# Kernel optimization log

Measured on AMD Instinct MI355X. Metric: run time of the kernel, lower is better.

The kernel has to match this reference:

```python
import jax, jax.numpy as jnp
import numpy as np

N_EMBD = 1024
HIDDEN = 4 * N_EMBD          # 4096
ADAPT = HIDDEN // 16         # 256
NUM_EXPERTS = 8
B, S = 4, 2048
LN_EPS = 1e-5


def setup_inputs() -> dict:
    key = jax.random.key(0)
    ks = jax.random.split(key, 8)
    x = jax.random.normal(ks[0], (B, S, N_EMBD), dtype=jnp.float32)
    # top-1 routing: one-hot expert weights (disjoint masks, standard MoE dispatch)
    route = jax.random.randint(ks[1], (B, S), 0, NUM_EXPERTS)
    expert_weights = jax.nn.one_hot(route, NUM_EXPERTS, dtype=jnp.float32)
    up_scale = 0.1 / N_EMBD ** 0.5
    adapt_scale0 = 0.1 / HIDDEN ** 0.5
    adapt_scale = 0.01 / ADAPT ** 0.5
    W_up = jax.random.normal(ks[2], (HIDDEN, N_EMBD), dtype=jnp.float32) * up_scale
    W_adapt = jax.random.normal(ks[3], (ADAPT, HIDDEN), dtype=jnp.float32) * adapt_scale0
    W_exp_adapters = jax.random.normal(ks[4], (NUM_EXPERTS, ADAPT, ADAPT), dtype=jnp.float32) * adapt_scale
    ln_gamma = jnp.ones((NUM_EXPERTS, ADAPT), dtype=jnp.float32)
    ln_beta = jnp.zeros((NUM_EXPERTS, ADAPT), dtype=jnp.float32)
    W_expert_proj = jax.random.normal(ks[5], (HIDDEN, ADAPT), dtype=jnp.float32) * adapt_scale
    W_out = jax.random.normal(ks[6], (N_EMBD, HIDDEN), dtype=jnp.float32) * adapt_scale
    return {"x": x, "expert_weights": expert_weights, "W_up": W_up,
            "W_adapt": W_adapt, "W_exp_adapters": W_exp_adapters,
            "ln_gamma": ln_gamma, "ln_beta": ln_beta,
            "W_expert_proj": W_expert_proj, "W_out": W_out}


def reference(x, expert_weights, W_up, W_adapt, W_exp_adapters, ln_gamma, ln_beta, W_expert_proj, W_out):
    b, s, d = x.shape
    T = b * s
    E = expert_weights.shape[-1]
    xt = x.reshape(T, d)

    # shared MLP path (silu(up_proj(x))) -> output_proj
    h = jax.nn.silu(xt @ W_up.T)                      # [T, HIDDEN]
    shared_out = (h @ W_out.T).reshape(b, s, d)       # [B, S, D]

    active = expert_weights.reshape(T, E) > 0         # [T, E]
    any_active = jnp.any(active, axis=-1)             # [T]
    last_idx = E - 1 - jnp.argmax(active[:, ::-1], axis=-1)  # [T]

    # pre_adapt (silu(up) recomputed == h) -> adapt_proj
    a = h @ W_adapt.T                                 # [T, ADAPT]
    # per-expert adapter linears, then select the winning expert per token
    a_all = jnp.einsum('td,eod->teo', a, W_exp_adapters)      # [T, E, ADAPT]
    a_sel = jnp.take_along_axis(a_all, last_idx[:, None, None], axis=1)[:, 0]  # [T, ADAPT]

    # per-expert LayerNorm params gathered per token
    g = ln_gamma[last_idx]                            # [T, ADAPT]
    be = ln_beta[last_idx]
    mu = jnp.mean(a_sel, axis=-1, keepdims=True)
    var = jnp.mean(jnp.square(a_sel - mu), axis=-1, keepdims=True)
    a_norm = (a_sel - mu) * jax.lax.rsqrt(var + LN_EPS) * g + be

    h2 = a_norm @ W_expert_proj.T                     # [T, HIDDEN]
    e_out = h2 @ W_out.T                              # [T, D]
    combined = jnp.where(any_active[:, None], e_out, 0.0).reshape(b, s, d)
    return shared_out + 0.1 * combined
```

## Files before the change

### kernel.cpp

```cpp
#include <hip/hip_runtime.h>
#include <cstdint>

#define TOK  8192
#define DEMB 1024
#define HID  4096
#define ADP  256
#define NEXP 8
#define KAUG 4352

typedef __bf16 bf16x8 __attribute__((ext_vector_type(8)));
typedef float  f32x4  __attribute__((ext_vector_type(4)));

__device__ __forceinline__ unsigned short f2bf(float f) {
  unsigned int u = __float_as_uint(f);
  u += 0x7fffu + ((u >> 16) & 1u);
  return (unsigned short)(u >> 16);
}
__device__ __forceinline__ float bf2f(unsigned short b) {
  return __uint_as_float(((unsigned int)b) << 16);
}

__global__ __launch_bounds__(256) void convert_all(
    const float* __restrict__ x, const float* __restrict__ wup,
    const float* __restrict__ wout, const float* __restrict__ wadapt,
    const float* __restrict__ wexp, const float* __restrict__ ew,
    unsigned short* __restrict__ xb, unsigned short* __restrict__ wub,
    unsigned short* __restrict__ wob, unsigned short* __restrict__ wab,
    unsigned short* __restrict__ web, int* __restrict__ route) {
  int b = blockIdx.x;
  if (b >= 8960) {
    int t = (b - 8960) * 256 + threadIdx.x;
    const float* p = ew + (size_t)t * NEXP;
    int r = -1;
#pragma unroll
    for (int e = 0; e < NEXP; ++e)
      if (p[e] > 0.f) r = e;
    route[t] = r;
    return;
  }
  const float* src; unsigned short* dst; int lb; bool strided = false;
  if      (b < 4096) { src = x;      dst = xb;  lb = b; }
  else if (b < 6144) { src = wup;    dst = wub; lb = b - 4096; }
  else if (b < 8192) { src = wout;   dst = wob; lb = b - 6144; strided = true; }
  else if (b < 8704) { src = wadapt; dst = wab; lb = b - 8192; }
  else               { src = wexp;   dst = web; lb = b - 8704; }
  size_t base = (size_t)lb * 2048;
#pragma unroll
  for (int h = 0; h < 2; ++h) {
    size_t off = base + (size_t)h * 1024 + (size_t)threadIdx.x * 4;
    float4 v = *(const float4*)(src + off);
    ushort4 o;
    o.x = f2bf(v.x); o.y = f2bf(v.y); o.z = f2bf(v.z); o.w = f2bf(v.w);
    size_t doff = strided ? (off >> 12) * KAUG + (off & 4095) : off;
    *(ushort4*)(dst + doff) = o;
  }
}

__global__ __launch_bounds__(256) void wp_transpose(
    const float* __restrict__ wp, unsigned short* __restrict__ wpT) {
  __shared__ float tile[64][65];
  const int h0 = blockIdx.x * 64;
  const int a0 = blockIdx.y * 64;
  const int t = threadIdx.x;
  const int r = t >> 4;
  const int c = (t & 15) * 4;
#pragma unroll
  for (int p = 0; p < 4; ++p) {
    int row = p * 16 + r;
    float4 v = *(const float4*)(wp + (size_t)(h0 + row) * ADP + a0 + c);
    tile[c + 0][row] = v.x;
    tile[c + 1][row] = v.y;
    tile[c + 2][row] = v.z;
    tile[c + 3][row] = v.w;
  }
  __syncthreads();
#pragma unroll
  for (int q = 0; q < 2; ++q) {
    int idx = q * 256 + t;
    int al = idx >> 3;
    int hg = (idx & 7) * 8;
    unsigned int w0 = (unsigned int)f2bf(tile[al][hg + 0]) |
                      ((unsigned int)f2bf(tile[al][hg + 1]) << 16);
    unsigned int w1 = (unsigned int)f2bf(tile[al][hg + 2]) |
                      ((unsigned int)f2bf(tile[al][hg + 3]) << 16);
    unsigned int w2 = (unsigned int)f2bf(tile[al][hg + 4]) |
                      ((unsigned int)f2bf(tile[al][hg + 5]) << 16);
    unsigned int w3 = (unsigned int)f2bf(tile[al][hg + 6]) |
                      ((unsigned int)f2bf(tile[al][hg + 7]) << 16);
    uint4 o = make_uint4(w0, w1, w2, w3);
    *(uint4*)(wpT + (size_t)(a0 + al) * HID + h0 + hg) = o;
  }
}

__device__ __forceinline__ void stage_tile(const unsigned short* __restrict__ g,
                                           int ldg, unsigned short* lds,
                                           int wave, int lane) {
  int srow = lane >> 3;
  int scol = ((lane & 7) ^ (srow & 7)) * 8;
#pragma unroll
  for (int c = 0; c < 4; ++c) {
    int chunk = wave * 4 + c;
    const unsigned short* gp = g + (size_t)(chunk * 8 + srow) * ldg + scol;
    unsigned short* lp = lds + chunk * 512;
    __builtin_amdgcn_global_load_lds(
        (const __attribute__((address_space(1))) unsigned int*)(uintptr_t)gp,
        (__attribute__((address_space(3))) unsigned int*)(uintptr_t)lp,
        16, 0, 0);
  }
}

template <int EPI>
__global__ __launch_bounds__(256) void gemm128(
    const unsigned short* __restrict__ A, int lda,
    const unsigned short* __restrict__ B, int ldb,
    void* __restrict__ C, int ldc,
    const int* __restrict__ route, int kLen, long splitStride) {
  __shared__ unsigned short As[128 * 64];
  __shared__ unsigned short Bs[128 * 64];
  const int lane = threadIdx.x & 63;
  const int wave = threadIdx.x >> 6;
  const int wm = wave >> 1, wn = wave & 1;
  const long rowBase = (long)blockIdx.y * 128;
  const long colBase = (long)blockIdx.x * 128;
  const int ks = blockIdx.z * kLen;
  const unsigned short* Ap = A + rowBase * lda + ks;
  const unsigned short* Bp = B + colBase * ldb + ks;
  f32x4 acc[4][4] = {};

  for (int kt = 0; kt < kLen; kt += 64) {
    stage_tile(Ap + kt, lda, As, wave, lane);
    stage_tile(Bp + kt, ldb, Bs, wave, lane);
    __syncthreads();
#pragma unroll
    for (int kk = 0; kk < 64; kk += 32) {
      const int kb = (kk >> 3) + (lane >> 4);
      const int sw = kb ^ (lane & 7);
      bf16x8 af[4], bfr[4];
#pragma unroll
      for (int mt = 0; mt < 4; ++mt) {
        int m = wm * 64 + mt * 16 + (lane & 15);
        af[mt] = *(const bf16x8*)&As[m * 64 + sw * 8];
      }
#pragma unroll
      for (int nt = 0; nt < 4; ++nt) {
        int n = wn * 64 + nt * 16 + (lane & 15);
        bfr[nt] = *(const bf16x8*)&Bs[n * 64 + sw * 8];
      }
#pragma unroll
      for (int mt = 0; mt < 4; ++mt)
#pragma unroll
        for (int nt = 0; nt < 4; ++nt)
          acc[mt][nt] = __builtin_amdgcn_mfma_f32_16x16x32_bf16(
              af[mt], bfr[nt], acc[mt][nt], 0, 0, 0);
    }
    __syncthreads();
  }

  const int rsub = (lane >> 4) * 4;
  const int csub = lane & 15;
#pragma unroll
  for (int mt = 0; mt < 4; ++mt) {
#pragma unroll
    for (int nt = 0; nt < 4; ++nt) {
      long col = colBase + wn * 64 + nt * 16 + csub;
#pragma unroll
      for (int r = 0; r < 4; ++r) {
        long row = rowBase + wm * 64 + mt * 16 + rsub + r;
        float v = acc[mt][nt][r];
        if (EPI == 0) {
          float s = __fdividef(v, 1.0f + __expf(-v));
          ((unsigned short*)C)[row * ldc + col] = f2bf(s);
        } else if (EPI == 1) {
          ((float*)C + splitStride * blockIdx.z)[row * ldc + col] = v;
        } else {
          if (route[row] == (int)(col >> 8))
            ((float*)C)[row * ADP + (col & 255)] = v;
        }
      }
    }
  }
}

__global__ __launch_bounds__(256) void reduce_cast(
    const float* __restrict__ P, unsigned short* __restrict__ ab) {
  size_t i = ((size_t)blockIdx.x * 256 + threadIdx.x) * 4;
  const size_t stride = (size_t)TOK * ADP;
  float4 p0 = *(const float4*)(P + i);
  float4 p1 = *(const float4*)(P + stride + i);
  float4 p2 = *(const float4*)(P + 2 * stride + i);
  float4 p3 = *(const float4*)(P + 3 * stride + i);
  ushort4 o;
  o.x = f2bf(p0.x + p1.x + p2.x + p3.x);
  o.y = f2bf(p0.y + p1.y + p2.y + p3.y);
  o.z = f2bf(p0.z + p1.z + p2.z + p3.z);
  o.w = f2bf(p0.w + p1.w + p2.w + p3.w);
  *(ushort4*)(ab + i) = o;
}

__global__ __launch_bounds__(256) void wcomb_reduce(
    const float* __restrict__ Pw, unsigned short* __restrict__ wob) {
  size_t i = ((size_t)blockIdx.x * 256 + threadIdx.x) * 4;
  const size_t stride = (size_t)DEMB * ADP;
  float4 s = *(const float4*)(Pw + i);
#pragma unroll
  for (int k = 1; k < 8; ++k) {
    float4 p = *(const float4*)(Pw + k * stride + i);
    s.x += p.x; s.y += p.y; s.z += p.z; s.w += p.w;
  }
  size_t d = i >> 8, a = i & 255;
  ushort4 o;
  o.x = f2bf(0.1f * s.x); o.y = f2bf(0.1f * s.y);
  o.z = f2bf(0.1f * s.z); o.w = f2bf(0.1f * s.w);
  *(ushort4*)(wob + d * KAUG + HID + a) = o;
}

__global__ __launch_bounds__(256) void ln_kernel(
    const float* __restrict__ asel, const int* __restrict__ route,
    const float* __restrict__ gamma, const float* __restrict__ beta,
    unsigned short* __restrict__ haug) {
  const int lane = threadIdx.x & 63;
  const int t = blockIdx.x * 4 + (threadIdx.x >> 6);
  const int e = route[t];
  float4 v = *(const float4*)(asel + (size_t)t * ADP + lane * 4);
  float s1 = v.x + v.y + v.z + v.w;
  float s2 = v.x * v.x + v.y * v.y + v.z * v.z + v.w * v.w;
#pragma unroll
  for (int off = 32; off > 0; off >>= 1) {
    s1 += __shfl_down(s1, off);
    s2 += __shfl_down(s2, off);
  }
  s1 = __shfl(s1, 0);
  s2 = __shfl(s2, 0);
  float mu = s1 * (1.0f / ADP);
  float var = s2 * (1.0f / ADP) - mu * mu;
  float rstd = rsqrtf(var + 1e-5f);
  ushort4 o;
  if (e >= 0) {
    float4 g = *(const float4*)(gamma + (size_t)e * ADP + lane * 4);
    float4 b = *(const float4*)(beta + (size_t)e * ADP + lane * 4);
    o.x = f2bf((v.x - mu) * rstd * g.x + b.x);
    o.y = f2bf((v.y - mu) * rstd * g.y + b.y);
    o.z = f2bf((v.z - mu) * rstd * g.z + b.z);
    o.w = f2bf((v.w - mu) * rstd * g.w + b.w);
  } else {
    o.x = o.y = o.z = o.w = 0;
  }
  *(ushort4*)(haug + (size_t)t * KAUG + HID + lane * 4) = o;
}

extern "C" void kernel_launch(void* const* d_in, const int* in_sizes, int n_in,
                              void* d_out, int out_size, void* d_ws, size_t ws_size,
                              hipStream_t stream) {
  const float* x     = (const float*)d_in[0];
  const float* ew    = (const float*)d_in[1];
  const float* W_up  = (const float*)d_in[2];
  const float* W_ad  = (const float*)d_in[3];
  const float* W_ex  = (const float*)d_in[4];
  const float* gam   = (const float*)d_in[5];
  const float* bet   = (const float*)d_in[6];
  const float* W_pr  = (const float*)d_in[7];
  const float* W_out = (const float*)d_in[8];
  float* out = (float*)d_out;

  char* ws = (char*)d_ws;
  size_t off = 0;
  auto alloc = [&](size_t n) {
    char* p = ws + off;
    off += (n + 255) & ~(size_t)255;
    return p;
  };
  unsigned short* xb   = (unsigned short*)alloc((size_t)TOK * DEMB * 2);
  unsigned short* wub  = (unsigned short*)alloc((size_t)HID * DEMB * 2);
  unsigned short* wob  = (unsigned short*)alloc((size_t)DEMB * KAUG * 2);
  unsigned short* wab  = (unsigned short*)alloc((size_t)ADP * HID * 2);
  unsigned short* web  = (unsigned short*)alloc((size_t)NEXP * ADP * ADP * 2);
  unsigned short* wpT  = (unsigned short*)alloc((size_t)ADP * HID * 2);
  unsigned short* Haug = (unsigned short*)alloc((size_t)TOK * KAUG * 2);
  float*          P    = (float*)alloc((size_t)4 * TOK * ADP * 4);
  float*          Pw   = (float*)alloc((size_t)8 * DEMB * ADP * 4);
  unsigned short* ab   = (unsigned short*)alloc((size_t)TOK * ADP * 2);
  int*          route  = (int*)alloc((size_t)TOK * 4);
  float* asel = P;

  convert_all<<<8992, 256, 0, stream>>>(x, W_up, W_out, W_ad, W_ex, ew,
                                        xb, wub, wob, wab, web, route);
  wp_transpose<<<dim3(HID / 64, ADP / 64), 256, 0, stream>>>(W_pr, wpT);
  gemm128<1><<<dim3(ADP / 128, DEMB / 128, 8), 256, 0, stream>>>(
      wob, KAUG, wpT, HID, Pw, ADP, nullptr, HID / 8, (long)DEMB * ADP);
  wcomb_reduce<<<DEMB * ADP / 1024, 256, 0, stream>>>(Pw, wob);
  gemm128<0><<<dim3(HID / 128, TOK / 128, 1), 256, 0, stream>>>(
      xb, DEMB, wub, DEMB, Haug, KAUG, nullptr, DEMB, 0);
  gemm128<1><<<dim3(ADP / 128, TOK / 128, 4), 256, 0, stream>>>(
      Haug, KAUG, wab, HID, P, ADP, nullptr, HID / 4, (long)TOK * ADP);
  reduce_cast<<<TOK * ADP / 1024, 256, 0, stream>>>(P, ab);
  gemm128<3><<<dim3(NEXP * ADP / 128, TOK / 128, 1), 256, 0, stream>>>(
      ab, ADP, web, ADP, asel, ADP, route, ADP, 0);
  ln_kernel<<<TOK / 4, 256, 0, stream>>>(asel, route, gam, bet, Haug);
  gemm128<1><<<dim3(DEMB / 128, TOK / 128, 1), 256, 0, stream>>>(
      Haug, KAUG, wob, KAUG, out, DEMB, nullptr, KAUG, 0);
}
```

Measured before the change: 399.6 us.

## Merge small kernels into fused launches and remap GEMM blocks per XCD

Folds the W_proj transpose into the conversion kernel and runs the W_out·W_proj combine GEMM in the same launch as the adapt-projection split-K GEMM. The two split-K reductions are likewise merged into one kernel. GEMM block indices are remapped so adjacent row tiles land on the same XCD, which should improve L2 reuse, and launch bounds now request 3 blocks per CU. The goal is fewer launches and less tail idle time, at the cost of branchier kernels and the shared-memory tile now being allocated in every conversion block.

```diff
diff --git a/kernel.cpp b/kernel.cpp
--- a/kernel.cpp
+++ b/kernel.cpp
@@ -24,10 +24,48 @@
     const float* __restrict__ x, const float* __restrict__ wup,
     const float* __restrict__ wout, const float* __restrict__ wadapt,
     const float* __restrict__ wexp, const float* __restrict__ ew,
+    const float* __restrict__ wp,
     unsigned short* __restrict__ xb, unsigned short* __restrict__ wub,
     unsigned short* __restrict__ wob, unsigned short* __restrict__ wab,
-    unsigned short* __restrict__ web, int* __restrict__ route) {
+    unsigned short* __restrict__ web, int* __restrict__ route,
+    unsigned short* __restrict__ wpT) {
+  __shared__ float tile[64][65];
   int b = blockIdx.x;
+  if (b >= 8992) {
+    int wli = b - 8992;
+    const int h0 = (wli & 63) * 64;
+    const int a0 = (wli >> 6) * 64;
+    const int t = threadIdx.x;
+    const int r = t >> 4;
+    const int c = (t & 15) * 4;
+#pragma unroll
+    for (int p = 0; p < 4; ++p) {
+      int row = p * 16 + r;
+      float4 v = *(const float4*)(wp + (size_t)(h0 + row) * ADP + a0 + c);
+      tile[c + 0][row] = v.x;
+      tile[c + 1][row] = v.y;
+      tile[c + 2][row] = v.z;
+      tile[c + 3][row] = v.w;
+    }
+    __syncthreads();
+#pragma unroll
+    for (int q = 0; q < 2; ++q) {
+      int idx = q * 256 + t;
+      int al = idx >> 3;
+      int hg = (idx & 7) * 8;
+      unsigned int w0 = (unsigned int)f2bf(tile[al][hg + 0]) |
+                        ((unsigned int)f2bf(tile[al][hg + 1]) << 16);
+      unsigned int w1 = (unsigned int)f2bf(tile[al][hg + 2]) |
+                        ((unsigned int)f2bf(tile[al][hg + 3]) << 16);
+      unsigned int w2 = (unsigned int)f2bf(tile[al][hg + 4]) |
+                        ((unsigned int)f2bf(tile[al][hg + 5]) << 16);
+      unsigned int w3 = (unsigned int)f2bf(tile[al][hg + 6]) |
+                        ((unsigned int)f2bf(tile[al][hg + 7]) << 16);
+      *(uint4*)(wpT + (size_t)(a0 + al) * HID + h0 + hg) =
+          make_uint4(w0, w1, w2, w3);
+    }
+    return;
+  }
   if (b >= 8960) {
     int t = (b - 8960) * 256 + threadIdx.x;
     const float* p = ew + (size_t)t * NEXP;
@@ -53,42 +91,6 @@
     o.x = f2bf(v.x); o.y = f2bf(v.y); o.z = f2bf(v.z); o.w = f2bf(v.w);
     size_t doff = strided ? (off >> 12) * KAUG + (off & 4095) : off;
     *(ushort4*)(dst + doff) = o;
-  }
-}
-
-__global__ __launch_bounds__(256) void wp_transpose(
-    const float* __restrict__ wp, unsigned short* __restrict__ wpT) {
-  __shared__ float tile[64][65];
-  const int h0 = blockIdx.x * 64;
-  const int a0 = blockIdx.y * 64;
-  const int t = threadIdx.x;
-  const int r = t >> 4;
-  const int c = (t & 15) * 4;
-#pragma unroll
-  for (int p = 0; p < 4; ++p) {
-    int row = p * 16 + r;
-    float4 v = *(const float4*)(wp + (size_t)(h0 + row) * ADP + a0 + c);
-    tile[c + 0][row] = v.x;
-    tile[c + 1][row] = v.y;
-    tile[c + 2][row] = v.z;
-    tile[c + 3][row] = v.w;
-  }
-  __syncthreads();
-#pragma unroll
-  for (int q = 0; q < 2; ++q) {
-    int idx = q * 256 + t;
-    int al = idx >> 3;
-    int hg = (idx & 7) * 8;
-    unsigned int w0 = (unsigned int)f2bf(tile[al][hg + 0]) |
-                      ((unsigned int)f2bf(tile[al][hg + 1]) << 16);
-    unsigned int w1 = (unsigned int)f2bf(tile[al][hg + 2]) |
-                      ((unsigned int)f2bf(tile[al][hg + 3]) << 16);
-    unsigned int w2 = (unsigned int)f2bf(tile[al][hg + 4]) |
-                      ((unsigned int)f2bf(tile[al][hg + 5]) << 16);
-    unsigned int w3 = (unsigned int)f2bf(tile[al][hg + 6]) |
-                      ((unsigned int)f2bf(tile[al][hg + 7]) << 16);
-    uint4 o = make_uint4(w0, w1, w2, w3);
-    *(uint4*)(wpT + (size_t)(a0 + al) * HID + h0 + hg) = o;
   }
 }
 
@@ -109,20 +111,28 @@
   }
 }
 
+__device__ __forceinline__ void remap_xcd(int li, int gx, int gy,
+                                          int& bx, int& by) {
+  int xcd = li & 7;
+  int slot = li >> 3;
+  bx = slot % gx;
+  by = xcd * (gy >> 3) + slot / gx;
+}
+
 template <int EPI>
-__global__ __launch_bounds__(256) void gemm128(
+__device__ __forceinline__ void gemm_body(
+    int bxr, int byr, int bz,
     const unsigned short* __restrict__ A, int lda,
     const unsigned short* __restrict__ B, int ldb,
     void* __restrict__ C, int ldc,
-    const int* __restrict__ route, int kLen, long splitStride) {
-  __shared__ unsigned short As[128 * 64];
-  __shared__ unsigned short Bs[128 * 64];
+    const int* __restrict__ route, int kLen, long splitStride,
+    unsigned short* As, unsigned short* Bs) {
   const int lane = threadIdx.x & 63;
   const int wave = threadIdx.x >> 6;
   const int wm = wave >> 1, wn = wave & 1;
-  const long rowBase = (long)blockIdx.y * 128;
-  const long colBase = (long)blockIdx.x * 128;
-  const int ks = blockIdx.z * kLen;
+  const long rowBase = (long)byr * 128;
+  const long colBase = (long)bxr * 128;
+  const int ks = bz * kLen;
   const unsigned short* Ap = A + rowBase * lda + ks;
   const unsigned short* Bp = B + colBase * ldb + ks;
   f32x4 acc[4][4] = {};
@@ -171,7 +181,7 @@
           float s = __fdividef(v, 1.0f + __expf(-v));
           ((unsigned short*)C)[row * ldc + col] = f2bf(s);
         } else if (EPI == 1) {
-          ((float*)C + splitStride * blockIdx.z)[row * ldc + col] = v;
+          ((float*)C + splitStride * bz)[row * ldc + col] = v;
         } else {
           if (route[row] == (int)(col >> 8))
             ((float*)C)[row * ADP + (col & 255)] = v;
@@ -181,37 +191,82 @@
   }
 }
 
-__global__ __launch_bounds__(256) void reduce_cast(
-    const float* __restrict__ P, unsigned short* __restrict__ ab) {
-  size_t i = ((size_t)blockIdx.x * 256 + threadIdx.x) * 4;
-  const size_t stride = (size_t)TOK * ADP;
-  float4 p0 = *(const float4*)(P + i);
-  float4 p1 = *(const float4*)(P + stride + i);
-  float4 p2 = *(const float4*)(P + 2 * stride + i);
-  float4 p3 = *(const float4*)(P + 3 * stride + i);
-  ushort4 o;
-  o.x = f2bf(p0.x + p1.x + p2.x + p3.x);
-  o.y = f2bf(p0.y + p1.y + p2.y + p3.y);
-  o.z = f2bf(p0.z + p1.z + p2.z + p3.z);
-  o.w = f2bf(p0.w + p1.w + p2.w + p3.w);
-  *(ushort4*)(ab + i) = o;
-}
-
-__global__ __launch_bounds__(256) void wcomb_reduce(
+template <int EPI>
+__global__ __launch_bounds__(256, 3) void gemm128(
+    const unsigned short* __restrict__ A, int lda,
+    const unsigned short* __restrict__ B, int ldb,
+    void* __restrict__ C, int ldc,
+    const int* __restrict__ route, int kLen, long splitStride) {
+  __shared__ unsigned short As[128 * 64];
+  __shared__ unsigned short Bs[128 * 64];
+  int li = blockIdx.x + gridDim.x * blockIdx.y;
+  int bx, by;
+  remap_xcd(li, gridDim.x, gridDim.y, bx, by);
+  gemm_body<EPI>(bx, by, blockIdx.z, A, lda, B, ldb, C, ldc, route, kLen,
+                 splitStride, As, Bs);
+}
+
+__global__ __launch_bounds__(256, 3) void gemm_dual(
+    const unsigned short* __restrict__ A0, int lda0,
+    const unsigned short* __restrict__ B0, int ldb0,
+    float* __restrict__ C0, int ldc0, int kLen0, long ss0, int gx0, int gy0,
+    int nb0,
+    const unsigned short* __restrict__ A1, int lda1,
+    const unsigned short* __restrict__ B1, int ldb1,
+    float* __restrict__ C1, int ldc1, int kLen1, long ss1, int gx1, int gy1) {
+  __shared__ unsigned short As[128 * 64];
+  __shared__ unsigned short Bs[128 * 64];
+  int li = blockIdx.x;
+  if (li < nb0) {
+    int per = gx0 * gy0;
+    int z = li / per, rem = li % per;
+    int bx, by;
+    remap_xcd(rem, gx0, gy0, bx, by);
+    gemm_body<1>(bx, by, z, A0, lda0, B0, ldb0, C0, ldc0, nullptr, kLen0, ss0,
+                 As, Bs);
+  } else {
+    int wli = li - nb0;
+    int per = gx1 * gy1;
+    int z = wli / per, rem = wli % per;
+    int bx, by;
+    remap_xcd(rem, gx1, gy1, bx, by);
+    gemm_body<1>(bx, by, z, A1, lda1, B1, ldb1, C1, ldc1, nullptr, kLen1, ss1,
+                 As, Bs);
+  }
+}
+
+__global__ __launch_bounds__(256) void reduce_both(
+    const float* __restrict__ P, unsigned short* __restrict__ ab,
     const float* __restrict__ Pw, unsigned short* __restrict__ wob) {
-  size_t i = ((size_t)blockIdx.x * 256 + threadIdx.x) * 4;
-  const size_t stride = (size_t)DEMB * ADP;
-  float4 s = *(const float4*)(Pw + i);
-#pragma unroll
-  for (int k = 1; k < 8; ++k) {
-    float4 p = *(const float4*)(Pw + k * stride + i);
-    s.x += p.x; s.y += p.y; s.z += p.z; s.w += p.w;
-  }
-  size_t d = i >> 8, a = i & 255;
-  ushort4 o;
-  o.x = f2bf(0.1f * s.x); o.y = f2bf(0.1f * s.y);
-  o.z = f2bf(0.1f * s.z); o.w = f2bf(0.1f * s.w);
-  *(ushort4*)(wob + d * KAUG + HID + a) = o;
+  int b = blockIdx.x;
+  if (b < 2048) {
+    size_t i = ((size_t)b * 256 + threadIdx.x) * 4;
+    const size_t stride = (size_t)TOK * ADP;
+    float4 p0 = *(const float4*)(P + i);
+    float4 p1 = *(const float4*)(P + stride + i);
+    float4 p2 = *(const float4*)(P + 2 * stride + i);
+    float4 p3 = *(const float4*)(P + 3 * stride + i);
+    ushort4 o;
+    o.x = f2bf(p0.x + p1.x + p2.x + p3.x);
+    o.y = f2bf(p0.y + p1.y + p2.y + p3.y);
+    o.z = f2bf(p0.z + p1.z + p2.z + p3.z);
+    o.w = f2bf(p0.w + p1.w + p2.w + p3.w);
+    *(ushort4*)(ab + i) = o;
+  } else {
+    size_t i = ((size_t)(b - 2048) * 256 + threadIdx.x) * 4;
+    const size_t stride = (size_t)DEMB * ADP;
+    float4 s = *(const float4*)(Pw + i);
+#pragma unroll
+    for (int k = 1; k < 8; ++k) {
+      float4 p = *(const float4*)(Pw + k * stride + i);
+      s.x += p.x; s.y += p.y; s.z += p.z; s.w += p.w;
+    }
+    size_t d = i >> 8, a = i & 255;
+    ushort4 o;
+    o.x = f2bf(0.1f * s.x); o.y = f2bf(0.1f * s.y);
+    o.z = f2bf(0.1f * s.z); o.w = f2bf(0.1f * s.w);
+    *(ushort4*)(wob + d * KAUG + HID + a) = o;
+  }
 }
 
 __global__ __launch_bounds__(256) void ln_kernel(
@@ -282,17 +337,14 @@
   int*          route  = (int*)alloc((size_t)TOK * 4);
   float* asel = P;
 
-  convert_all<<<8992, 256, 0, stream>>>(x, W_up, W_out, W_ad, W_ex, ew,
-                                        xb, wub, wob, wab, web, route);
-  wp_transpose<<<dim3(HID / 64, ADP / 64), 256, 0, stream>>>(W_pr, wpT);
-  gemm128<1><<<dim3(ADP / 128, DEMB / 128, 8), 256, 0, stream>>>(
-      wob, KAUG, wpT, HID, Pw, ADP, nullptr, HID / 8, (long)DEMB * ADP);
-  wcomb_reduce<<<DEMB * ADP / 1024, 256, 0, stream>>>(Pw, wob);
+  convert_all<<<9248, 256, 0, stream>>>(x, W_up, W_out, W_ad, W_ex, ew, W_pr,
+                                        xb, wub, wob, wab, web, route, wpT);
   gemm128<0><<<dim3(HID / 128, TOK / 128, 1), 256, 0, stream>>>(
       xb, DEMB, wub, DEMB, Haug, KAUG, nullptr, DEMB, 0);
-  gemm128<1><<<dim3(ADP / 128, TOK / 128, 4), 256, 0, stream>>>(
-      Haug, KAUG, wab, HID, P, ADP, nullptr, HID / 4, (long)TOK * ADP);
-  reduce_cast<<<TOK * ADP / 1024, 256, 0, stream>>>(P, ab);
+  gemm_dual<<<640, 256, 0, stream>>>(
+      Haug, KAUG, wab, HID, P, ADP, HID / 4, (long)TOK * ADP, 2, 64, 512,
+      wob, KAUG, wpT, HID, Pw, ADP, HID / 8, (long)DEMB * ADP, 2, 8);
+  reduce_both<<<2304, 256, 0, stream>>>(P, ab, Pw, wob);
   gemm128<3><<<dim3(NEXP * ADP / 128, TOK / 128, 1), 256, 0, stream>>>(
       ab, ADP, web, ADP, asel, ADP, route, ADP, 0);
   ln_kernel<<<TOK / 4, 256, 0, stream>>>(asel, route, gam, bet, Haug);
```

Result: faster. 346.2 us (-13.4%).

## Fuse all stages into one persistent kernel with grid barriers and XCD-aware tile mapping

Applied to the files above, without the earlier changes.

Replaces ten separate kernel launches with a single persistent kernel of 512 blocks that walks through the conversion, GEMM, reduction, LayerNorm and final GEMM stages, separated by atomic-counter grid barriers. GEMM tiles are remapped so that blocks sharing an XCD work on neighbouring row tiles, to improve L2 reuse. The small Pw GEMM now runs in the same phase as the adapt GEMM, so the two overlap. The intent is to remove launch gaps and tail effects between stages. In exchange, the barriers spin-wait and assume all 512 blocks are co-resident (launch bounds request 3 blocks per CU), which risks deadlock and leaves less parallelism in the large GEMM phases.

```diff
diff --git a/kernel.cpp b/kernel.cpp
--- a/kernel.cpp
+++ b/kernel.cpp
@@ -7,6 +7,7 @@
 #define ADP  256
 #define NEXP 8
 #define KAUG 4352
+#define NBLK 512
 
 typedef __bf16 bf16x8 __attribute__((ext_vector_type(8)));
 typedef float  f32x4  __attribute__((ext_vector_type(4)));
@@ -20,76 +21,17 @@
   return __uint_as_float(((unsigned int)b) << 16);
 }
 
-__global__ __launch_bounds__(256) void convert_all(
-    const float* __restrict__ x, const float* __restrict__ wup,
-    const float* __restrict__ wout, const float* __restrict__ wadapt,
-    const float* __restrict__ wexp, const float* __restrict__ ew,
-    unsigned short* __restrict__ xb, unsigned short* __restrict__ wub,
-    unsigned short* __restrict__ wob, unsigned short* __restrict__ wab,
-    unsigned short* __restrict__ web, int* __restrict__ route) {
-  int b = blockIdx.x;
-  if (b >= 8960) {
-    int t = (b - 8960) * 256 + threadIdx.x;
-    const float* p = ew + (size_t)t * NEXP;
-    int r = -1;
-#pragma unroll
-    for (int e = 0; e < NEXP; ++e)
-      if (p[e] > 0.f) r = e;
-    route[t] = r;
-    return;
-  }
-  const float* src; unsigned short* dst; int lb; bool strided = false;
-  if      (b < 4096) { src = x;      dst = xb;  lb = b; }
-  else if (b < 6144) { src = wup;    dst = wub; lb = b - 4096; }
-  else if (b < 8192) { src = wout;   dst = wob; lb = b - 6144; strided = true; }
-  else if (b < 8704) { src = wadapt; dst = wab; lb = b - 8192; }
-  else               { src = wexp;   dst = web; lb = b - 8704; }
-  size_t base = (size_t)lb * 2048;
-#pragma unroll
-  for (int h = 0; h < 2; ++h) {
-    size_t off = base + (size_t)h * 1024 + (size_t)threadIdx.x * 4;
-    float4 v = *(const float4*)(src + off);
-    ushort4 o;
-    o.x = f2bf(v.x); o.y = f2bf(v.y); o.z = f2bf(v.z); o.w = f2bf(v.w);
-    size_t doff = strided ? (off >> 12) * KAUG + (off & 4095) : off;
-    *(ushort4*)(dst + doff) = o;
-  }
-}
-
-__global__ __launch_bounds__(256) void wp_transpose(
-    const float* __restrict__ wp, unsigned short* __restrict__ wpT) {
-  __shared__ float tile[64][65];
-  const int h0 = blockIdx.x * 64;
-  const int a0 = blockIdx.y * 64;
-  const int t = threadIdx.x;
-  const int r = t >> 4;
-  const int c = (t & 15) * 4;
-#pragma unroll
-  for (int p = 0; p < 4; ++p) {
-    int row = p * 16 + r;
-    float4 v = *(const float4*)(wp + (size_t)(h0 + row) * ADP + a0 + c);
-    tile[c + 0][row] = v.x;
-    tile[c + 1][row] = v.y;
-    tile[c + 2][row] = v.z;
-    tile[c + 3][row] = v.w;
-  }
+__device__ __forceinline__ void grid_bar(int* bar, int target) {
   __syncthreads();
-#pragma unroll
-  for (int q = 0; q < 2; ++q) {
-    int idx = q * 256 + t;
-    int al = idx >> 3;
-    int hg = (idx & 7) * 8;
-    unsigned int w0 = (unsigned int)f2bf(tile[al][hg + 0]) |
-                      ((unsigned int)f2bf(tile[al][hg + 1]) << 16);
-    unsigned int w1 = (unsigned int)f2bf(tile[al][hg + 2]) |
-                      ((unsigned int)f2bf(tile[al][hg + 3]) << 16);
-    unsigned int w2 = (unsigned int)f2bf(tile[al][hg + 4]) |
-                      ((unsigned int)f2bf(tile[al][hg + 5]) << 16);
-    unsigned int w3 = (unsigned int)f2bf(tile[al][hg + 6]) |
-                      ((unsigned int)f2bf(tile[al][hg + 7]) << 16);
-    uint4 o = make_uint4(w0, w1, w2, w3);
-    *(uint4*)(wpT + (size_t)(a0 + al) * HID + h0 + hg) = o;
-  }
+  if (threadIdx.x == 0) {
+    __threadfence();
+    __hip_atomic_fetch_add(bar, 1, __ATOMIC_ACQ_REL, __HIP_MEMORY_SCOPE_AGENT);
+    while (__hip_atomic_load(bar, __ATOMIC_ACQUIRE, __HIP_MEMORY_SCOPE_AGENT) <
+           target)
+      __builtin_amdgcn_s_sleep(2);
+    __threadfence();
+  }
+  __syncthreads();
 }
 
 __device__ __forceinline__ void stage_tile(const unsigned short* __restrict__ g,
@@ -109,20 +51,28 @@
   }
 }
 
+__device__ __forceinline__ void remap_xcd(int li, int gx, int gy,
+                                          int& bx, int& by) {
+  int xcd = li & 7;
+  int slot = li >> 3;
+  bx = slot % gx;
+  by = xcd * (gy >> 3) + slot / gx;
+}
+
 template <int EPI>
-__global__ __launch_bounds__(256) void gemm128(
+__device__ __forceinline__ void gemm_body(
+    int bxr, int byr, int bz,
     const unsigned short* __restrict__ A, int lda,
     const unsigned short* __restrict__ B, int ldb,
     void* __restrict__ C, int ldc,
-    const int* __restrict__ route, int kLen, long splitStride) {
-  __shared__ unsigned short As[128 * 64];
-  __shared__ unsigned short Bs[128 * 64];
+    const int* __restrict__ route, int kLen, long splitStride,
+    unsigned short* As, unsigned short* Bs) {
   const int lane = threadIdx.x & 63;
   const int wave = threadIdx.x >> 6;
   const int wm = wave >> 1, wn = wave & 1;
-  const long rowBase = (long)blockIdx.y * 128;
-  const long colBase = (long)blockIdx.x * 128;
-  const int ks = blockIdx.z * kLen;
+  const long rowBase = (long)byr * 128;
+  const long colBase = (long)bxr * 128;
+  const int ks = bz * kLen;
   const unsigned short* Ap = A + rowBase * lda + ks;
   const unsigned short* Bp = B + colBase * ldb + ks;
   f32x4 acc[4][4] = {};
@@ -171,7 +121,7 @@
           float s = __fdividef(v, 1.0f + __expf(-v));
           ((unsigned short*)C)[row * ldc + col] = f2bf(s);
         } else if (EPI == 1) {
-          ((float*)C + splitStride * blockIdx.z)[row * ldc + col] = v;
+          ((float*)C + splitStride * bz)[row * ldc + col] = v;
         } else {
           if (route[row] == (int)(col >> 8))
             ((float*)C)[row * ADP + (col & 255)] = v;
@@ -181,71 +131,185 @@
   }
 }
 
-__global__ __launch_bounds__(256) void reduce_cast(
-    const float* __restrict__ P, unsigned short* __restrict__ ab) {
-  size_t i = ((size_t)blockIdx.x * 256 + threadIdx.x) * 4;
-  const size_t stride = (size_t)TOK * ADP;
-  float4 p0 = *(const float4*)(P + i);
-  float4 p1 = *(const float4*)(P + stride + i);
-  float4 p2 = *(const float4*)(P + 2 * stride + i);
-  float4 p3 = *(const float4*)(P + 3 * stride + i);
-  ushort4 o;
-  o.x = f2bf(p0.x + p1.x + p2.x + p3.x);
-  o.y = f2bf(p0.y + p1.y + p2.y + p3.y);
-  o.z = f2bf(p0.z + p1.z + p2.z + p3.z);
-  o.w = f2bf(p0.w + p1.w + p2.w + p3.w);
-  *(ushort4*)(ab + i) = o;
-}
-
-__global__ __launch_bounds__(256) void wcomb_reduce(
-    const float* __restrict__ Pw, unsigned short* __restrict__ wob) {
-  size_t i = ((size_t)blockIdx.x * 256 + threadIdx.x) * 4;
-  const size_t stride = (size_t)DEMB * ADP;
-  float4 s = *(const float4*)(Pw + i);
-#pragma unroll
-  for (int k = 1; k < 8; ++k) {
-    float4 p = *(const float4*)(Pw + k * stride + i);
-    s.x += p.x; s.y += p.y; s.z += p.z; s.w += p.w;
-  }
-  size_t d = i >> 8, a = i & 255;
-  ushort4 o;
-  o.x = f2bf(0.1f * s.x); o.y = f2bf(0.1f * s.y);
-  o.z = f2bf(0.1f * s.z); o.w = f2bf(0.1f * s.w);
-  *(ushort4*)(wob + d * KAUG + HID + a) = o;
-}
-
-__global__ __launch_bounds__(256) void ln_kernel(
-    const float* __restrict__ asel, const int* __restrict__ route,
-    const float* __restrict__ gamma, const float* __restrict__ beta,
-    unsigned short* __restrict__ haug) {
-  const int lane = threadIdx.x & 63;
-  const int t = blockIdx.x * 4 + (threadIdx.x >> 6);
-  const int e = route[t];
-  float4 v = *(const float4*)(asel + (size_t)t * ADP + lane * 4);
-  float s1 = v.x + v.y + v.z + v.w;
-  float s2 = v.x * v.x + v.y * v.y + v.z * v.z + v.w * v.w;
-#pragma unroll
-  for (int off = 32; off > 0; off >>= 1) {
-    s1 += __shfl_down(s1, off);
-    s2 += __shfl_down(s2, off);
-  }
-  s1 = __shfl(s1, 0);
-  s2 = __shfl(s2, 0);
-  float mu = s1 * (1.0f / ADP);
-  float var = s2 * (1.0f / ADP) - mu * mu;
-  float rstd = rsqrtf(var + 1e-5f);
-  ushort4 o;
-  if (e >= 0) {
-    float4 g = *(const float4*)(gamma + (size_t)e * ADP + lane * 4);
-    float4 b = *(const float4*)(beta + (size_t)e * ADP + lane * 4);
-    o.x = f2bf((v.x - mu) * rstd * g.x + b.x);
-    o.y = f2bf((v.y - mu) * rstd * g.y + b.y);
-    o.z = f2bf((v.z - mu) * rstd * g.z + b.z);
-    o.w = f2bf((v.w - mu) * rstd * g.w + b.w);
-  } else {
-    o.x = o.y = o.z = o.w = 0;
-  }
-  *(ushort4*)(haug + (size_t)t * KAUG + HID + lane * 4) = o;
+__global__ __launch_bounds__(256, 3) void fused_all(
+    const float* __restrict__ x, const float* __restrict__ ew,
+    const float* __restrict__ wup, const float* __restrict__ wadapt,
+    const float* __restrict__ wexp, const float* __restrict__ gamma,
+    const float* __restrict__ beta, const float* __restrict__ wp,
+    const float* __restrict__ wout,
+    unsigned short* __restrict__ xb, unsigned short* __restrict__ wub,
+    unsigned short* __restrict__ wob, unsigned short* __restrict__ wab,
+    unsigned short* __restrict__ web, unsigned short* __restrict__ wpT,
+    unsigned short* __restrict__ Haug, float* __restrict__ P,
+    float* __restrict__ Pw, unsigned short* __restrict__ ab,
+    int* __restrict__ route, float* __restrict__ out, int* bar) {
+  __shared__ unsigned char smem[32768];
+  unsigned short* As = (unsigned short*)smem;
+  unsigned short* Bs = (unsigned short*)(smem + 16384);
+  const int b = blockIdx.x;
+  const int xcd = b & 7, slot = b >> 3;
+  const int tid = threadIdx.x;
+
+  for (int u = b; u < 9248; u += NBLK) {
+    if (u >= 8992) {
+      float (*tile)[65] = (float(*)[65])smem;
+      int wli = u - 8992;
+      const int h0 = (wli & 63) * 64;
+      const int a0 = (wli >> 6) * 64;
+      const int r = tid >> 4;
+      const int c = (tid & 15) * 4;
+      __syncthreads();
+#pragma unroll
+      for (int p = 0; p < 4; ++p) {
+        int row = p * 16 + r;
+        float4 v = *(const float4*)(wp + (size_t)(h0 + row) * ADP + a0 + c);
+        tile[c + 0][row] = v.x;
+        tile[c + 1][row] = v.y;
+        tile[c + 2][row] = v.z;
+        tile[c + 3][row] = v.w;
+      }
+      __syncthreads();
+#pragma unroll
+      for (int q = 0; q < 2; ++q) {
+        int idx = q * 256 + tid;
+        int al = idx >> 3;
+        int hg = (idx & 7) * 8;
+        unsigned int w0 = (unsigned int)f2bf(tile[al][hg + 0]) |
+                          ((unsigned int)f2bf(tile[al][hg + 1]) << 16);
+        unsigned int w1 = (unsigned int)f2bf(tile[al][hg + 2]) |
+                          ((unsigned int)f2bf(tile[al][hg + 3]) << 16);
+        unsigned int w2 = (unsigned int)f2bf(tile[al][hg + 4]) |
+                          ((unsigned int)f2bf(tile[al][hg + 5]) << 16);
+        unsigned int w3 = (unsigned int)f2bf(tile[al][hg + 6]) |
+                          ((unsigned int)f2bf(tile[al][hg + 7]) << 16);
+        *(uint4*)(wpT + (size_t)(a0 + al) * HID + h0 + hg) =
+            make_uint4(w0, w1, w2, w3);
+      }
+    } else if (u >= 8960) {
+      int t = (u - 8960) * 256 + tid;
+      const float* p = ew + (size_t)t * NEXP;
+      int r = -1;
+#pragma unroll
+      for (int e = 0; e < NEXP; ++e)
+        if (p[e] > 0.f) r = e;
+      route[t] = r;
+    } else {
+      const float* src; unsigned short* dst; int lb; bool strided = false;
+      if      (u < 4096) { src = x;      dst = xb;  lb = u; }
+      else if (u < 6144) { src = wup;    dst = wub; lb = u - 4096; }
+      else if (u < 8192) { src = wout;   dst = wob; lb = u - 6144; strided = true; }
+      else if (u < 8704) { src = wadapt; dst = wab; lb = u - 8192; }
+      else               { src = wexp;   dst = web; lb = u - 8704; }
+      size_t base = (size_t)lb * 2048;
+#pragma unroll
+      for (int h = 0; h < 2; ++h) {
+        size_t off = base + (size_t)h * 1024 + (size_t)tid * 4;
+        float4 v = *(const float4*)(src + off);
+        ushort4 o;
+        o.x = f2bf(v.x); o.y = f2bf(v.y); o.z = f2bf(v.z); o.w = f2bf(v.w);
+        size_t doff = strided ? (off >> 12) * KAUG + (off & 4095) : off;
+        *(ushort4*)(dst + doff) = o;
+      }
+    }
+  }
+  grid_bar(bar, NBLK);
+
+#pragma unroll 1
+  for (int i = 0; i < 4; ++i) {
+    int s = slot + i * 64;
+    gemm_body<0>(s & 31, xcd * 8 + (s >> 5), 0, xb, DEMB, wub, DEMB, Haug,
+                 KAUG, nullptr, DEMB, 0, As, Bs);
+  }
+  grid_bar(bar, 2 * NBLK);
+
+  {
+    int z = b >> 7, rem = b & 127, bx, by;
+    remap_xcd(rem, 2, 64, bx, by);
+    gemm_body<1>(bx, by, z, Haug, KAUG, wab, HID, P, ADP, nullptr, HID / 4,
+                 (long)TOK * ADP, As, Bs);
+    if (b < 128) {
+      int z2 = b >> 4, rem2 = b & 15, cx, cy;
+      remap_xcd(rem2, 2, 8, cx, cy);
+      gemm_body<1>(cx, cy, z2, wob, KAUG, wpT, HID, Pw, ADP, nullptr, HID / 8,
+                   (long)DEMB * ADP, As, Bs);
+    }
+  }
+  grid_bar(bar, 3 * NBLK);
+
+  for (int u = b; u < 2304; u += NBLK) {
+    if (u < 2048) {
+      size_t i = ((size_t)u * 256 + tid) * 4;
+      const size_t stride = (size_t)TOK * ADP;
+      float4 p0 = *(const float4*)(P + i);
+      float4 p1 = *(const float4*)(P + stride + i);
+      float4 p2 = *(const float4*)(P + 2 * stride + i);
+      float4 p3 = *(const float4*)(P + 3 * stride + i);
+      ushort4 o;
+      o.x = f2bf(p0.x + p1.x + p2.x + p3.x);
+      o.y = f2bf(p0.y + p1.y + p2.y + p3.y);
+      o.z = f2bf(p0.z + p1.z + p2.z + p3.z);
+      o.w = f2bf(p0.w + p1.w + p2.w + p3.w);
+      *(ushort4*)(ab + i) = o;
+    } else {
+      size_t i = ((size_t)(u - 2048) * 256 + tid) * 4;
+      const size_t stride = (size_t)DEMB * ADP;
+      float4 s = *(const float4*)(Pw + i);
+#pragma unroll
+      for (int k = 1; k < 8; ++k) {
+        float4 p = *(const float4*)(Pw + k * stride + i);
+        s.x += p.x; s.y += p.y; s.z += p.z; s.w += p.w;
+      }
+      size_t d = i >> 8, a = i & 255;
+      ushort4 o;
+      o.x = f2bf(0.1f * s.x); o.y = f2bf(0.1f * s.y);
+      o.z = f2bf(0.1f * s.z); o.w = f2bf(0.1f * s.w);
+      *(ushort4*)(wob + d * KAUG + HID + a) = o;
+    }
+  }
+  grid_bar(bar, 4 * NBLK);
+
+#pragma unroll 1
+  for (int i = 0; i < 2; ++i) {
+    int s = slot + i * 64;
+    gemm_body<3>(s & 15, xcd * 8 + (s >> 4), 0, ab, ADP, web, ADP, P, ADP,
+                 route, ADP, 0, As, Bs);
+  }
+  grid_bar(bar, 5 * NBLK);
+
+  for (int u = b; u < 2048; u += NBLK) {
+    const int lane = tid & 63;
+    const int t = u * 4 + (tid >> 6);
+    const int e = route[t];
+    float4 v = *(const float4*)(P + (size_t)t * ADP + lane * 4);
+    float s1 = v.x + v.y + v.z + v.w;
+    float s2 = v.x * v.x + v.y * v.y + v.z * v.z + v.w * v.w;
+#pragma unroll
+    for (int off = 32; off > 0; off >>= 1) {
+      s1 += __shfl_down(s1, off);
+      s2 += __shfl_down(s2, off);
+    }
+    s1 = __shfl(s1, 0);
+    s2 = __shfl(s2, 0);
+    float mu = s1 * (1.0f / ADP);
+    float var = s2 * (1.0f / ADP) - mu * mu;
+    float rstd = rsqrtf(var + 1e-5f);
+    ushort4 o;
+    if (e >= 0) {
+      float4 g = *(const float4*)(gamma + (size_t)e * ADP + lane * 4);
+      float4 bb = *(const float4*)(beta + (size_t)e * ADP + lane * 4);
+      o.x = f2bf((v.x - mu) * rstd * g.x + bb.x);
+      o.y = f2bf((v.y - mu) * rstd * g.y + bb.y);
+      o.z = f2bf((v.z - mu) * rstd * g.z + bb.z);
+      o.w = f2bf((v.w - mu) * rstd * g.w + bb.w);
+    } else {
+      o.x = o.y = o.z = o.w = 0;
+    }
+    *(ushort4*)(Haug + (size_t)t * KAUG + HID + lane * 4) = o;
+  }
+  grid_bar(bar, 6 * NBLK);
+
+  gemm_body<1>(slot & 7, xcd * 8 + (slot >> 3), 0, Haug, KAUG, wob, KAUG, out,
+               DEMB, nullptr, KAUG, 0, As, Bs);
 }
 
 extern "C" void kernel_launch(void* const* d_in, const int* in_sizes, int n_in,
@@ -269,6 +333,7 @@
     off += (n + 255) & ~(size_t)255;
     return p;
   };
+  int*          bar    = (int*)alloc(256);
   unsigned short* xb   = (unsigned short*)alloc((size_t)TOK * DEMB * 2);
   unsigned short* wub  = (unsigned short*)alloc((size_t)HID * DEMB * 2);
   unsigned short* wob  = (unsigned short*)alloc((size_t)DEMB * KAUG * 2);
@@ -280,22 +345,9 @@
   float*          Pw   = (float*)alloc((size_t)8 * DEMB * ADP * 4);
   unsigned short* ab   = (unsigned short*)alloc((size_t)TOK * ADP * 2);
   int*          route  = (int*)alloc((size_t)TOK * 4);
-  float* asel = P;
-
-  convert_all<<<8992, 256, 0, stream>>>(x, W_up, W_out, W_ad, W_ex, ew,
-                                        xb, wub, wob, wab, web, route);
-  wp_transpose<<<dim3(HID / 64, ADP / 64), 256, 0, stream>>>(W_pr, wpT);
-  gemm128<1><<<dim3(ADP / 128, DEMB / 128, 8), 256, 0, stream>>>(
-      wob, KAUG, wpT, HID, Pw, ADP, nullptr, HID / 8, (long)DEMB * ADP);
-  wcomb_reduce<<<DEMB * ADP / 1024, 256, 0, stream>>>(Pw, wob);
-  gemm128<0><<<dim3(HID / 128, TOK / 128, 1), 256, 0, stream>>>(
-      xb, DEMB, wub, DEMB, Haug, KAUG, nullptr, DEMB, 0);
-  gemm128<1><<<dim3(ADP / 128, TOK / 128, 4), 256, 0, stream>>>(
-      Haug, KAUG, wab, HID, P, ADP, nullptr, HID / 4, (long)TOK * ADP);
-  reduce_cast<<<TOK * ADP / 1024, 256, 0, stream>>>(P, ab);
-  gemm128<3><<<dim3(NEXP * ADP / 128, TOK / 128, 1), 256, 0, stream>>>(
-      ab, ADP, web, ADP, asel, ADP, route, ADP, 0);
-  ln_kernel<<<TOK / 4, 256, 0, stream>>>(asel, route, gam, bet, Haug);
-  gemm128<1><<<dim3(DEMB / 128, TOK / 128, 1), 256, 0, stream>>>(
-      Haug, KAUG, wob, KAUG, out, DEMB, nullptr, KAUG, 0);
-}
+
+  hipMemsetAsync(bar, 0, 4, stream);
+  fused_all<<<NBLK, 256, 0, stream>>>(x, ew, W_up, W_ad, W_ex, gam, bet, W_pr,
+                                      W_out, xb, wub, wob, wab, web, wpT, Haug,
+                                      P, Pw, ab, route, out, bar);
+}
```

Result: slower. 817.6 us (+104.6%).
